# Performance work log

Hardware: AMD Instinct MI355X
Metric: run time of the kernel (lower is better)

The kernel has to match this reference:

```python
import jax, jax.numpy as jnp
import numpy as np

B, C, H, W = 64, 512, 8, 8
K = 100            # num_class
H1, HID, L = 64, 128, 32   # ae_hidden[0], fixed hidd, ae_latent
CLIP = 100.0       # CSSRClassifier.clip_len
RED = -0.1         # model='pcssr' -> -1, times gamma=0.1
PUSH_THRESH = 10000.0


def setup_inputs() -> dict:
    key = jax.random.key(0)
    ks = jax.random.split(key, 9)
    s = lambda fan_in: 1.0 / np.sqrt(fan_in)  # kaiming-ish 1x1 conv init scale
    return {
        "x": jax.random.normal(ks[0], (B, C, H, W), jnp.float32),
        "ycls": jax.random.randint(ks[1], (B,), 0, K),
        "safe_margin_all": jax.random.normal(ks[2], (K,), jnp.float32),
        "safe_distance_all": jax.random.normal(ks[3], (K,), jnp.float32),
        "W1": jax.random.normal(ks[4], (K, H1, C), jnp.float32) * s(C),
        "W2": jax.random.normal(ks[5], (K, HID, H1), jnp.float32) * s(H1),
        "W3": jax.random.normal(ks[6], (K, L, HID), jnp.float32) * s(HID),
        "prototypes": jax.random.normal(ks[7], (K, L, H, W), jnp.float32),
        "prototypes1": jax.random.normal(ks[8], (K, L, H, W), jnp.float32),
    }


def reference(x, ycls, safe_margin_all, safe_distance_all, W1, W2, W3, prototypes, prototypes1):
    P = H * W
    xf = x.reshape(B, C, P)
    # per-class 1x1-conv encoder (tanh after every conv), batched over classes k
    h = jnp.tanh(jnp.einsum('koc,bcp->kbop', W1, xf))      # [K,B,H1,P]
    h = jnp.tanh(jnp.einsum('koi,kbip->kbop', W2, h))      # [K,B,HID,P]
    lt = jnp.tanh(jnp.einsum('koi,kbip->kbop', W3, h))     # [K,B,L,P]
    p = prototypes.reshape(K, 1, L, P)
    p1 = prototypes1.reshape(K, 1, L, P)
    # squared-L2 distance over channel dim, scaled by reduction, clipped
    er = jnp.clip(jnp.sum((lt - p) ** 2, axis=2) * RED, -CLIP, CLIP)    # [K,B,P]
    er1 = jnp.clip(jnp.sum((lt - p1) ** 2, axis=2) * RED, -CLIP, CLIP)  # [K,B,P]
    # training losses (pull on er1, push on er), vectorized across classes
    f = jnp.sum(er, axis=2)    # [K,B] spatial-summed errors
    f1 = jnp.sum(er1, axis=2)  # [K,B]
    cls_ids = jnp.arange(K)[:, None]
    mask_eq = (ycls[None, :] == cls_ids).astype(f.dtype)   # [K,B]
    n_eq = jnp.sum(mask_eq, axis=1)
    pull = jnp.sum(jnp.where(n_eq > 0,
                             jnp.sum(f1 * mask_eq, axis=1) / jnp.maximum(n_eq, 1.0),
                             0.0))
    comb = (1.0 - mask_eq) * (f < PUSH_THRESH).astype(f.dtype)
    n_comb = jnp.sum(comb, axis=1)
    push = jnp.sum(jnp.where(n_comb > 0,
                             jnp.sum(f * comb, axis=1) / jnp.maximum(n_comb, 1.0),
                             0.0))
    # cat per-class [B,1,H,W] errors along dim 1 -> [B,K,H,W]
    logits = jnp.transpose(er, (1, 0, 2)).reshape(B, K, H, W)
    logits1 = jnp.transpose(er1, (1, 0, 2)).reshape(B, K, H, W)
    return logits, logits1, pull, push
```

## Files before the change

kernel.cpp:

```cpp
#include <hip/hip_runtime.h>

typedef short  s16x8  __attribute__((ext_vector_type(8)));
typedef float  f32x16 __attribute__((ext_vector_type(16)));
typedef unsigned short u16;
typedef unsigned long long u64b;

#define MFMA32(a,b,c) __builtin_amdgcn_mfma_f32_32x32x16_bf16((a),(b),(c),0,0,0)
#define KCLS 100

__device__ __forceinline__ u16 f2bf(float f) {
  return (u16)(__builtin_bit_cast(unsigned, f) >> 16);
}

__device__ __forceinline__ float tanh_fast(float x) {
  float e = __builtin_amdgcn_exp2f(x * 2.8853900817779268f);
  return 1.0f - 2.0f * __builtin_amdgcn_rcpf(e + 1.0f);
}

__device__ __forceinline__ void ld_lds16(const void* g, void* l) {
  __builtin_amdgcn_global_load_lds(
      (const __attribute__((address_space(1))) unsigned char*)g,
      (__attribute__((address_space(3))) unsigned char*)l, 16, 0, 0);
}

__global__ void prep(const float* __restrict__ x, const float* __restrict__ w1,
                     const float* __restrict__ w2, const float* __restrict__ w3,
                     u16* __restrict__ xF, u16* __restrict__ W1F,
                     u16* __restrict__ W2F, u16* __restrict__ W3F,
                     float* __restrict__ fz, float* __restrict__ out2) {
  __shared__ float tile[64][65];
  const int bid = blockIdx.x, t = threadIdx.x;
  if (bid == 0 && t < 2) out2[t] = 0.f;
  if (bid < 512) {
    const int b = bid >> 3, ck = bid & 7;
    #pragma unroll
    for (int j = 0; j < 4; j++) {
      int e4 = j * 1024 + t * 4;
      int c = e4 >> 6, p0 = e4 & 63;
      float4 v = *(const float4*)(x + ((size_t)b * 512 + ck * 64 + c) * 64 + p0);
      tile[c][p0] = v.x; tile[c][p0 + 1] = v.y; tile[c][p0 + 2] = v.z; tile[c][p0 + 3] = v.w;
    }
    __syncthreads();
    #pragma unroll
    for (int i = 0; i < 2; i++) {
      int s = i * 256 + t;
      int ksl = s >> 7, ph = (s >> 6) & 1, lane = s & 63;
      int cb = ksl * 16 + (lane >> 5) * 8, pp = ph * 32 + (lane & 31);
      u16 o[8];
      #pragma unroll
      for (int jj = 0; jj < 8; jj++) o[jj] = f2bf(tile[cb + jj][pp]);
      *(uint4*)(xF + (((size_t)b * 64 + (ck * 4 + ksl) * 2 + ph) * 512) + lane * 8) = *(uint4*)o;
    }
  } else if (bid < 1312) {
    int base = (bid - 512) * 512;
    #pragma unroll
    for (int i = 0; i < 2; i++) {
      int s = base + i * 256 + t;
      int frag = s >> 6, lane = s & 63;
      int k = frag >> 6, fr = frag & 63;
      int m = (fr & 1) * 32 + (lane & 31);
      int c0 = (fr >> 1) * 16 + (lane >> 5) * 8;
      const float* src = w1 + ((size_t)k * 64 + m) * 512 + c0;
      float4 a = *(const float4*)src, b4 = *(const float4*)(src + 4);
      u16 o[8] = { f2bf(a.x), f2bf(a.y), f2bf(a.z), f2bf(a.w),
                   f2bf(b4.x), f2bf(b4.y), f2bf(b4.z), f2bf(b4.w) };
      *(uint4*)(W1F + ((size_t)frag * 512) + lane * 8) = *(uint4*)o;
    }
  } else if (bid < 1512) {
    int base = (bid - 1312) * 512;
    #pragma unroll
    for (int i = 0; i < 2; i++) {
      int s = base + i * 256 + t;
      int frag = s >> 6, lane = s & 63;
      int k = frag >> 4, fr = frag & 15;
      int m = (fr & 3) * 32 + (lane & 31);
      int c0 = (fr >> 2) * 16 + (lane >> 5) * 8;
      const float* src = w2 + ((size_t)k * 128 + m) * 64 + c0;
      float4 a = *(const float4*)src, b4 = *(const float4*)(src + 4);
      u16 o[8] = { f2bf(a.x), f2bf(a.y), f2bf(a.z), f2bf(a.w),
                   f2bf(b4.x), f2bf(b4.y), f2bf(b4.z), f2bf(b4.w) };
      *(uint4*)(W2F + ((size_t)frag * 512) + lane * 8) = *(uint4*)o;
    }
  } else if (bid < 1612) {
    int base = (bid - 1512) * 512;
    #pragma unroll
    for (int i = 0; i < 2; i++) {
      int s = base + i * 256 + t;
      int frag = s >> 6, lane = s & 63;
      int k = frag >> 3, kb = frag & 7;
      int m = lane & 31;
      int c0 = kb * 16 + (lane >> 5) * 8;
      const float* src = w3 + ((size_t)k * 32 + m) * 128 + c0;
      float4 a = *(const float4*)src, b4 = *(const float4*)(src + 4);
      u16 o[8] = { f2bf(a.x), f2bf(a.y), f2bf(a.z), f2bf(a.w),
                   f2bf(b4.x), f2bf(b4.y), f2bf(b4.z), f2bf(b4.w) };
      *(uint4*)(W3F + ((size_t)frag * 512) + lane * 8) = *(uint4*)o;
    }
  } else {
    int i4 = (bid - 1612) * 256 + t;
    if (i4 < 3200) {
      float4 z = {0.f, 0.f, 0.f, 0.f};
      *(float4*)(fz + (size_t)i4 * 4) = z;
    }
  }
}

__global__ __launch_bounds__(256, 4) void cssr_main(
    const u16* __restrict__ W1F, const u16* __restrict__ W2F, const u16* __restrict__ W3F,
    const u16* __restrict__ xF, const float* __restrict__ protos,
    const float* __restrict__ protos1, float* __restrict__ out,
    float* __restrict__ fw, float* __restrict__ f1w)
{
  __shared__ u16 pool[16384];

  const int bid = blockIdx.x;
  const int kp = bid >> 6, b = bid & 63;
  const int tid = threadIdx.x, w = tid >> 6, lane = tid & 63;
  const int nhalf = lane >> 5, nn = lane & 31;
  const int kk = w >> 1, mt = w & 1;
  const int k = kp * 2 + kk;

  const u16* xb = xF + ((size_t)b * 64) * 512;

  #pragma unroll
  for (int i = 0; i < 4; i++) {
    int f = w * 4 + i, gksl = f >> 1, ph = f & 1;
    ld_lds16(xb + ((size_t)(gksl * 2 + ph)) * 512 + lane * 8, &pool[f * 512]);
  }
  __syncthreads();

  f32x16 acc1[2] = {};
  for (int ci = 0; ci < 4; ci++) {
    const int pb = ci & 1;
    if (ci < 3) {
      #pragma unroll
      for (int i = 0; i < 4; i++) {
        int f = w * 4 + i, gksl = f >> 1, ph = f & 1;
        ld_lds16(xb + ((size_t)(((ci + 1) * 8 + gksl) * 2 + ph)) * 512 + lane * 8,
                 &pool[(pb ^ 1) * 8192 + f * 512]);
      }
    }
    #pragma unroll
    for (int ksl = 0; ksl < 8; ksl++) {
      s16x8 A = *(const s16x8*)(W1F + (((size_t)k * 64 + (ci * 8 + ksl) * 2 + mt) * 512) + lane * 8);
      #pragma unroll
      for (int nt = 0; nt < 2; nt++) {
        s16x8 B = *(const s16x8*)&pool[pb * 8192 + (ksl * 2 + nt) * 512 + lane * 8];
        acc1[nt] = MFMA32(A, B, acc1[nt]);
      }
    }
    __syncthreads();
  }

  #pragma unroll
  for (int nt = 0; nt < 2; nt++) {
    #pragma unroll
    for (int g = 0; g < 4; g++) {
      u16 hv[4];
      #pragma unroll
      for (int q = 0; q < 4; q++) hv[q] = f2bf(tanh_fast(acc1[nt][g * 4 + q]));
      int kb = mt * 2 + (g >> 1);
      int tl = (g & 1) * 32 + nn;
      *(u64b*)&pool[kk * 4096 + (kb * 2 + nt) * 512 + tl * 8 + nhalf * 4] = *(u64b*)hv;
    }
  }
  __syncthreads();

  f32x16 acc2[2][2] = {};
  #pragma unroll
  for (int kb = 0; kb < 4; kb++) {
    s16x8 A0 = *(const s16x8*)(W2F + (((size_t)k * 16 + kb * 4 + mt * 2 + 0) * 512) + lane * 8);
    s16x8 A1 = *(const s16x8*)(W2F + (((size_t)k * 16 + kb * 4 + mt * 2 + 1) * 512) + lane * 8);
    #pragma unroll
    for (int nh = 0; nh < 2; nh++) {
      s16x8 B = *(const s16x8*)&pool[kk * 4096 + (kb * 2 + nh) * 512 + lane * 8];
      acc2[0][nh] = MFMA32(A0, B, acc2[0][nh]);
      acc2[1][nh] = MFMA32(A1, B, acc2[1][nh]);
    }
  }
  __syncthreads();

  #pragma unroll
  for (int m4l = 0; m4l < 2; m4l++) {
    #pragma unroll
    for (int nh = 0; nh < 2; nh++) {
      #pragma unroll
      for (int g = 0; g < 4; g++) {
        u16 hv[4];
        #pragma unroll
        for (int q = 0; q < 4; q++) hv[q] = f2bf(tanh_fast(acc2[m4l][nh][g * 4 + q]));
        int kb2 = mt * 4 + m4l * 2 + (g >> 1);
        int tl  = (g & 1) * 32 + nn;
        *(u64b*)&pool[kk * 8192 + (kb2 * 2 + nh) * 512 + tl * 8 + nhalf * 4] = *(u64b*)hv;
      }
    }
  }
  __syncthreads();

  f32x16 acc3 = {};
  #pragma unroll
  for (int kb = 0; kb < 8; kb++) {
    s16x8 A = *(const s16x8*)(W3F + (((size_t)k * 8 + kb) * 512) + lane * 8);
    s16x8 B = *(const s16x8*)&pool[kk * 8192 + (kb * 2 + mt) * 512 + lane * 8];
    acc3 = MFMA32(A, B, acc3);
  }

  const int p = mt * 32 + nn;
  const float* pr  = protos  + (size_t)k * 2048;
  const float* pr1 = protos1 + (size_t)k * 2048;
  float d2 = 0.f, d21 = 0.f;
  #pragma unroll
  for (int g = 0; g < 4; g++) {
    #pragma unroll
    for (int q = 0; q < 4; q++) {
      int m = q + 8 * g + 4 * nhalf;
      float lt = tanh_fast(acc3[g * 4 + q]);
      float d = lt - pr [m * 64 + p];  d2  += d * d;
      float e = lt - pr1[m * 64 + p];  d21 += e * e;
    }
  }
  d2 += __shfl_xor(d2, 32); d21 += __shfl_xor(d21, 32);
  float er  = fminf(fmaxf(d2  * -0.1f, -100.f), 100.f);
  float er1 = fminf(fmaxf(d21 * -0.1f, -100.f), 100.f);
  if (nhalf == 0) {
    out[(size_t)b * 6400 + k * 64 + p]          = er;
    out[409600 + (size_t)b * 6400 + k * 64 + p] = er1;
  }
  float s = er, s1 = er1;
  s += __shfl_xor(s, 1);  s1 += __shfl_xor(s1, 1);
  s += __shfl_xor(s, 2);  s1 += __shfl_xor(s1, 2);
  s += __shfl_xor(s, 4);  s1 += __shfl_xor(s1, 4);
  s += __shfl_xor(s, 8);  s1 += __shfl_xor(s1, 8);
  s += __shfl_xor(s, 16); s1 += __shfl_xor(s1, 16);
  if (lane == 0) {
    atomicAdd(&fw [k * 64 + b], s);
    atomicAdd(&f1w[k * 64 + b], s1);
  }
}

__global__ void finalize(const float* __restrict__ f, const float* __restrict__ f1,
                         const int* __restrict__ ycls, float* __restrict__ out2) {
  const int k = blockIdx.x, b = threadIdx.x;
  float fv = f[k * 64 + b], f1v = f1[k * 64 + b];
  bool eq = (ycls[b] == k);
  bool cb = (!eq) && (fv < 10000.f);
  float s1 = eq ? f1v : 0.f, ne = eq ? 1.f : 0.f;
  float s  = cb ? fv  : 0.f, nc = cb ? 1.f : 0.f;
  #pragma unroll
  for (int o = 1; o < 64; o <<= 1) {
    s1 += __shfl_xor(s1, o); ne += __shfl_xor(ne, o);
    s  += __shfl_xor(s,  o); nc += __shfl_xor(nc, o);
  }
  if (b == 0) {
    if (ne > 0.f) atomicAdd(&out2[0], s1 / ne);
    if (nc > 0.f) atomicAdd(&out2[1], s / nc);
  }
}

extern "C" void kernel_launch(void* const* d_in, const int* in_sizes, int n_in,
                              void* d_out, int out_size, void* d_ws, size_t ws_size,
                              hipStream_t stream) {
  const float* x     = (const float*)d_in[0];
  const int*   ycls  = (const int*)d_in[1];
  const float* W1    = (const float*)d_in[4];
  const float* W2    = (const float*)d_in[5];
  const float* W3    = (const float*)d_in[6];
  const float* prot  = (const float*)d_in[7];
  const float* prot1 = (const float*)d_in[8];
  float* out = (float*)d_out;

  char* ws = (char*)d_ws;
  u16*  xFb = (u16*)(ws);
  u16*  W1F = (u16*)(ws + 4194304);
  u16*  W2F = (u16*)(ws + 10747904);
  u16*  W3F = (u16*)(ws + 12386304);
  float* fw  = (float*)(ws + 13205504);
  float* f1w = (float*)(ws + 13231104);

  prep<<<1625, 256, 0, stream>>>(x, W1, W2, W3, xFb, W1F, W2F, W3F,
                                 fw, out + 819200);
  cssr_main<<<50 * 64, 256, 0, stream>>>(W1F, W2F, W3F, xFb, prot, prot1,
                                         out, fw, f1w);
  finalize<<<KCLS, 64, 0, stream>>>(fw, f1w, ycls, out + 819200);
}
```

Measured before the change: 143.3 us.

## Load whole x tile into LDS once, drop double-buffer syncs, pack bf16 with perm

Loads the full 64 KB bf16 x slice for the batch element into LDS up front instead of streaming four double-buffered chunks with a barrier after each. Layer-2 hidden activations move to a separate LDS region, which removes one barrier. bf16 packing now uses a byte-permute instruction. The larger LDS footprint lowers the occupancy hint from 4 to 2 blocks per CU, which may reduce latency hiding.

New measurement: 173.0 us. +20.8%, slower.

```diff
diff --git a/kernel.cpp b/kernel.cpp
--- a/kernel.cpp
+++ b/kernel.cpp
@@ -10,6 +10,14 @@
 
 __device__ __forceinline__ u16 f2bf(float f) {
   return (u16)(__builtin_bit_cast(unsigned, f) >> 16);
+}
+
+__device__ __forceinline__ unsigned pk2(float lo, float hi) {
+  return __builtin_amdgcn_perm(__builtin_bit_cast(unsigned, hi),
+                               __builtin_bit_cast(unsigned, lo), 0x07060302u);
+}
+__device__ __forceinline__ u64b pk4(float v0, float v1, float v2, float v3) {
+  return (u64b)pk2(v0, v1) | ((u64b)pk2(v2, v3) << 32);
 }
 
 __device__ __forceinline__ float tanh_fast(float x) {
@@ -105,13 +113,13 @@
   }
 }
 
-__global__ __launch_bounds__(256, 4) void cssr_main(
+__global__ __launch_bounds__(256, 2) void cssr_main(
     const u16* __restrict__ W1F, const u16* __restrict__ W2F, const u16* __restrict__ W3F,
     const u16* __restrict__ xF, const float* __restrict__ protos,
     const float* __restrict__ protos1, float* __restrict__ out,
     float* __restrict__ fw, float* __restrict__ f1w)
 {
-  __shared__ u16 pool[16384];
+  __shared__ u16 pool[40960];
 
   const int bid = blockIdx.x;
   const int kp = bid >> 6, b = bid & 63;
@@ -123,45 +131,32 @@
   const u16* xb = xF + ((size_t)b * 64) * 512;
 
   #pragma unroll
-  for (int i = 0; i < 4; i++) {
-    int f = w * 4 + i, gksl = f >> 1, ph = f & 1;
-    ld_lds16(xb + ((size_t)(gksl * 2 + ph)) * 512 + lane * 8, &pool[f * 512]);
+  for (int i = 0; i < 16; i++) {
+    int f = w * 16 + i;
+    ld_lds16(xb + (size_t)f * 512 + lane * 8, &pool[f * 512]);
   }
   __syncthreads();
 
   f32x16 acc1[2] = {};
-  for (int ci = 0; ci < 4; ci++) {
-    const int pb = ci & 1;
-    if (ci < 3) {
-      #pragma unroll
-      for (int i = 0; i < 4; i++) {
-        int f = w * 4 + i, gksl = f >> 1, ph = f & 1;
-        ld_lds16(xb + ((size_t)(((ci + 1) * 8 + gksl) * 2 + ph)) * 512 + lane * 8,
-                 &pool[(pb ^ 1) * 8192 + f * 512]);
-      }
-    }
-    #pragma unroll
-    for (int ksl = 0; ksl < 8; ksl++) {
-      s16x8 A = *(const s16x8*)(W1F + (((size_t)k * 64 + (ci * 8 + ksl) * 2 + mt) * 512) + lane * 8);
-      #pragma unroll
-      for (int nt = 0; nt < 2; nt++) {
-        s16x8 B = *(const s16x8*)&pool[pb * 8192 + (ksl * 2 + nt) * 512 + lane * 8];
-        acc1[nt] = MFMA32(A, B, acc1[nt]);
-      }
-    }
-    __syncthreads();
+  #pragma unroll 8
+  for (int g = 0; g < 32; g++) {
+    s16x8 A = *(const s16x8*)(W1F + (((size_t)k * 64 + g * 2 + mt) * 512) + lane * 8);
+    #pragma unroll
+    for (int nt = 0; nt < 2; nt++) {
+      s16x8 B = *(const s16x8*)&pool[(g * 2 + nt) * 512 + lane * 8];
+      acc1[nt] = MFMA32(A, B, acc1[nt]);
+    }
   }
 
   #pragma unroll
   for (int nt = 0; nt < 2; nt++) {
     #pragma unroll
     for (int g = 0; g < 4; g++) {
-      u16 hv[4];
-      #pragma unroll
-      for (int q = 0; q < 4; q++) hv[q] = f2bf(tanh_fast(acc1[nt][g * 4 + q]));
+      u64b hv = pk4(tanh_fast(acc1[nt][g * 4 + 0]), tanh_fast(acc1[nt][g * 4 + 1]),
+                    tanh_fast(acc1[nt][g * 4 + 2]), tanh_fast(acc1[nt][g * 4 + 3]));
       int kb = mt * 2 + (g >> 1);
       int tl = (g & 1) * 32 + nn;
-      *(u64b*)&pool[kk * 4096 + (kb * 2 + nt) * 512 + tl * 8 + nhalf * 4] = *(u64b*)hv;
+      *(u64b*)&pool[32768 + kk * 4096 + (kb * 2 + nt) * 512 + tl * 8 + nhalf * 4] = hv;
     }
   }
   __syncthreads();
@@ -173,25 +168,22 @@
     s16x8 A1 = *(const s16x8*)(W2F + (((size_t)k * 16 + kb * 4 + mt * 2 + 1) * 512) + lane * 8);
     #pragma unroll
     for (int nh = 0; nh < 2; nh++) {
-      s16x8 B = *(const s16x8*)&pool[kk * 4096 + (kb * 2 + nh) * 512 + lane * 8];
+      s16x8 B = *(const s16x8*)&pool[32768 + kk * 4096 + (kb * 2 + nh) * 512 + lane * 8];
       acc2[0][nh] = MFMA32(A0, B, acc2[0][nh]);
       acc2[1][nh] = MFMA32(A1, B, acc2[1][nh]);
     }
   }
-  __syncthreads();
-
   #pragma unroll
   for (int m4l = 0; m4l < 2; m4l++) {
     #pragma unroll
     for (int nh = 0; nh < 2; nh++) {
       #pragma unroll
       for (int g = 0; g < 4; g++) {
-        u16 hv[4];
-        #pragma unroll
-        for (int q = 0; q < 4; q++) hv[q] = f2bf(tanh_fast(acc2[m4l][nh][g * 4 + q]));
+        u64b hv = pk4(tanh_fast(acc2[m4l][nh][g * 4 + 0]), tanh_fast(acc2[m4l][nh][g * 4 + 1]),
+                      tanh_fast(acc2[m4l][nh][g * 4 + 2]), tanh_fast(acc2[m4l][nh][g * 4 + 3]));
         int kb2 = mt * 4 + m4l * 2 + (g >> 1);
         int tl  = (g & 1) * 32 + nn;
-        *(u64b*)&pool[kk * 8192 + (kb2 * 2 + nh) * 512 + tl * 8 + nhalf * 4] = *(u64b*)hv;
+        *(u64b*)&pool[kk * 8192 + (kb2 * 2 + nh) * 512 + tl * 8 + nhalf * 4] = hv;
       }
     }
   }
```
